# Performance work log

Hardware: AMD Instinct MI355X
Metric: run time of the kernel (lower is better)

## Reference

```python
import jax, jax.numpy as jnp
import numpy as np

EPS = 1e-5

def _layernorm(x, g, b):
    m = jnp.mean(x, axis=-1, keepdims=True)
    v = jnp.mean((x - m) ** 2, axis=-1, keepdims=True)
    return (x - m) * jax.lax.rsqrt(v + EPS) * g + b

def setup_inputs() -> dict:
    key = jax.random.key(0)
    ks = jax.random.split(key, 6)
    b, s, n = 1, 256, 512
    dim_msa, dim_pair, heads, dim_head = 64, 128, 8, 32
    dim_inner = heads * dim_head
    msa = jax.random.normal(ks[0], (b, s, n, dim_msa), dtype=jnp.float32)
    pairwise_repr = jax.random.normal(ks[1], (b, n, n, dim_pair), dtype=jnp.float32)
    mask = jnp.ones((b, n), dtype=bool)
    return {
        "msa": msa,
        "pairwise_repr": pairwise_repr,
        "ln_msa_g": jnp.ones((dim_msa,), jnp.float32),
        "ln_msa_b": jnp.zeros((dim_msa,), jnp.float32),
        "W_vg": jax.random.normal(ks[2], (dim_msa, dim_inner * 2), jnp.float32) * 0.02,
        "ln_pair_g": jnp.ones((dim_pair,), jnp.float32),
        "ln_pair_b": jnp.zeros((dim_pair,), jnp.float32),
        "W_pair": jax.random.normal(ks[3], (dim_pair, heads), jnp.float32) * 0.02,
        "W_out": jax.random.normal(ks[4], (dim_inner, dim_msa), jnp.float32) * 0.02,
        "mask": mask,
    }

def reference(msa, pairwise_repr, ln_msa_g, ln_msa_b, W_vg, ln_pair_g, ln_pair_b, W_pair, W_out, mask):
    heads, dim_head = 8, 32
    b, s, n, dim_msa = msa.shape
    # values and gates: LN -> LinearNoBias -> split (gv h d)
    vg = _layernorm(msa, ln_msa_g, ln_msa_b) @ W_vg            # [b,s,n,2*h*d]
    vg = vg.reshape(b, s, n, 2, heads, dim_head)
    vg = jnp.transpose(vg, (3, 0, 4, 1, 2, 5))                  # [2,b,h,s,n,d]
    values, gates = vg[0], jax.nn.sigmoid(vg[1])
    # pair bias: LN -> LinearNoBias -> [b,h,i,j]
    bias = _layernorm(pairwise_repr, ln_pair_g, ln_pair_b) @ W_pair  # [b,i,j,h]
    bias = jnp.transpose(bias, (0, 3, 1, 2))                    # [b,h,i,j]
    bias = jnp.where(mask[:, None, None, :], bias, -jnp.inf)
    weights = jax.nn.softmax(bias, axis=-1)                     # [b,h,i,j]
    out = jnp.einsum('bhij,bhsjd->bhsid', weights, values)      # [b,h,s,n,d]
    out = out * gates
    out = jnp.transpose(out, (0, 2, 3, 1, 4)).reshape(b, s, n, heads * dim_head)
    return out @ W_out                                          # [b,s,n,dim_msa]
```

## Files before the change

kernel.cpp:

```cpp
#include <hip/hip_runtime.h>
#include <hip/hip_bf16.h>


#define S 256
#define N 512
#define DM 64
#define DP 128
#define H 8
#define C 256
#define ROWS (S * N)

typedef __attribute__((ext_vector_type(8))) short bf16x8;
typedef __attribute__((ext_vector_type(4))) float f32x4;

static __device__ __forceinline__ float bf2f(unsigned int u16) {
    union { unsigned int i; float f; } x;
    x.i = u16 << 16;
    return x.f;
}
static __device__ __forceinline__ unsigned short f2bf(float f) {
    union { float f; unsigned int i; } x;
    x.f = f;
    unsigned int r = x.i + 0x7FFFu + ((x.i >> 16) & 1u);
    return (unsigned short)(r >> 16);
}
static __device__ __forceinline__ void gload16(const void* g, void* l) {
    __builtin_amdgcn_global_load_lds(
        (const __attribute__((address_space(1))) void*)g,
        (__attribute__((address_space(3))) void*)l, 16, 0, 0);
}

__global__ __launch_bounds__(256) void k0_prep(
    const float* __restrict__ Wvg, const float* __restrict__ g, const float* __restrict__ b,
    const float* __restrict__ Wout, const float* __restrict__ gp, const float* __restrict__ bp,
    const float* __restrict__ Wp,
    unsigned short* __restrict__ WTvg, float* __restrict__ biasvg, unsigned short* __restrict__ WoutT,
    float* __restrict__ Wg, float* __restrict__ sgcb)
{
    const int t = threadIdx.x;
    if (blockIdx.x < 2) {
        const int c = blockIdx.x * 256 + t;
        float bias = 0.f;
        unsigned short row[64];
#pragma unroll
        for (int k = 0; k < 64; k++) {
            const float w = Wvg[k * 512 + c];
            row[k] = f2bf(w * g[k]);
            bias = fmaf(w, b[k], bias);
        }
#pragma unroll
        for (int q = 0; q < 8; q++) *(uint4*)(WTvg + c * 64 + q * 8) = *(const uint4*)(row + q * 8);
        biasvg[c] = bias;
    } else if (blockIdx.x == 2) {
        const int m = t >> 2, c0 = (t & 3) * 64;
        unsigned short row[64];
#pragma unroll
        for (int q = 0; q < 64; q++) row[q] = f2bf(Wout[(c0 + q) * 64 + m]);
#pragma unroll
        for (int q = 0; q < 8; q++) *(uint4*)(WoutT + m * 256 + c0 + q * 8) = *(const uint4*)(row + q * 8);
    } else {
        if (t < 128) {
            const float gm = gp[t];
#pragma unroll
            for (int h = 0; h < 8; h++) Wg[t * 8 + h] = gm * Wp[t * 8 + h];
        } else if (t < 136) {
            const int h = t - 128;
            float sg = 0.f, cb = 0.f;
            for (int k = 0; k < 128; k++) {
                sg = fmaf(gp[k], Wp[k * 8 + h], sg);
                cb = fmaf(bp[k], Wp[k * 8 + h], cb);
            }
            sgcb[h] = sg;
            sgcb[8 + h] = cb;
        }
    }
}

__global__ __launch_bounds__(512, 4) void k1_vg_mfma(
    const float* __restrict__ msa, const unsigned short* __restrict__ WTvg,
    const float* __restrict__ biasvg,
    unsigned short* __restrict__ VT, unsigned short* __restrict__ G)
{
    __shared__ unsigned short wt[512 * 64];
    __shared__ unsigned short at[64 * 64];
    const int t = threadIdx.x, lane = t & 63, w = t >> 6;
    const int l15 = lane & 15, lgrp = lane >> 4;
    const int s = blockIdx.x >> 1;
    const int jbase = (blockIdx.x & 1) * 256;

#pragma unroll
    for (int q = 0; q < 8; q++) {
        const int u = q * 512 + t;
        const int c = u >> 3, ch = u & 7;
        const uint4 v = *(const uint4*)(WTvg + c * 64 + ch * 8);
        *(uint4*)((char*)wt + c * 128 + ((ch ^ (c & 7)) * 16)) = v;
    }
    float biasr[4];
    float bias2[4][4];
    if (w < 4) {
#pragma unroll
        for (int cf = 0; cf < 4; cf++) biasr[cf] = biasvg[w * 64 + cf * 16 + l15];
    } else {
#pragma unroll
        for (int cf = 0; cf < 4; cf++)
#pragma unroll
            for (int r = 0; r < 4; r++) bias2[cf][r] = biasvg[w * 64 + cf * 16 + lgrp * 4 + r];
    }

    for (int tile = 0; tile < 4; ++tile) {
        const int j0 = jbase + tile * 64;
        {
            const int r = t >> 3, kc = (t & 7) * 8;
            const float* src = msa + ((size_t)(s * 512 + j0 + r)) * 64 + kc;
            const float4 x0 = *(const float4*)src;
            const float4 x1 = *(const float4*)(src + 4);
            float s1 = x0.x + x0.y + x0.z + x0.w + x1.x + x1.y + x1.z + x1.w;
            float s2 = x0.x * x0.x + x0.y * x0.y + x0.z * x0.z + x0.w * x0.w
                     + x1.x * x1.x + x1.y * x1.y + x1.z * x1.z + x1.w * x1.w;
#pragma unroll
            for (int off = 1; off < 8; off <<= 1) {
                s1 += __shfl_xor(s1, off);
                s2 += __shfl_xor(s2, off);
            }
            const float m = s1 * (1.f / 64.f);
            const float inv = rsqrtf(s2 * (1.f / 64.f) - m * m + 1e-5f);
            unsigned short buf[8];
            buf[0] = f2bf((x0.x - m) * inv); buf[1] = f2bf((x0.y - m) * inv);
            buf[2] = f2bf((x0.z - m) * inv); buf[3] = f2bf((x0.w - m) * inv);
            buf[4] = f2bf((x1.x - m) * inv); buf[5] = f2bf((x1.y - m) * inv);
            buf[6] = f2bf((x1.z - m) * inv); buf[7] = f2bf((x1.w - m) * inv);
            *(uint4*)((char*)at + r * 128 + (((t & 7) ^ (r & 7)) * 16)) = *(const uint4*)buf;
        }
        __syncthreads();

        f32x4 acc[4][4];
#pragma unroll
        for (int rf = 0; rf < 4; rf++)
#pragma unroll
            for (int cf = 0; cf < 4; cf++) acc[rf][cf] = (f32x4){0.f, 0.f, 0.f, 0.f};

#pragma unroll
        for (int ks = 0; ks < 2; ks++) {
            bf16x8 bfr[4];
#pragma unroll
            for (int cf = 0; cf < 4; cf++) {
                const int c = w * 64 + cf * 16 + l15;
                bfr[cf] = *(const bf16x8*)((const char*)wt + c * 128 + (((ks * 4 + lgrp) ^ (c & 7)) * 16));
            }
#pragma unroll
            for (int rf = 0; rf < 4; rf++) {
                const int rr = rf * 16 + l15;
                const bf16x8 afr = *(const bf16x8*)((const char*)at + rr * 128 + (((ks * 4 + lgrp) ^ (rr & 7)) * 16));
                if (w < 4) {
#pragma unroll
                    for (int cf = 0; cf < 4; cf++)
                        acc[rf][cf] = __builtin_amdgcn_mfma_f32_16x16x32_bf16(afr, bfr[cf], acc[rf][cf], 0, 0, 0);
                } else {
#pragma unroll
                    for (int cf = 0; cf < 4; cf++)
                        acc[rf][cf] = __builtin_amdgcn_mfma_f32_16x16x32_bf16(bfr[cf], afr, acc[rf][cf], 0, 0, 0);
                }
            }
        }
        __syncthreads();

        if (w < 4) {
#pragma unroll
            for (int rf = 0; rf < 4; rf++)
#pragma unroll
                for (int cf = 0; cf < 4; cf++) {
                    const int c = w * 64 + cf * 16 + l15;
                    const int j = j0 + rf * 16 + lgrp * 4;
                    uint2 o;
                    o.x = (unsigned)f2bf(acc[rf][cf][0] + biasr[cf]) |
                          ((unsigned)f2bf(acc[rf][cf][1] + biasr[cf]) << 16);
                    o.y = (unsigned)f2bf(acc[rf][cf][2] + biasr[cf]) |
                          ((unsigned)f2bf(acc[rf][cf][3] + biasr[cf]) << 16);
                    *(uint2*)(VT + ((size_t)s * C + c) * N + j) = o;
                }
        } else {
#pragma unroll
            for (int rf = 0; rf < 4; rf++)
#pragma unroll
                for (int cf = 0; cf < 4; cf++) {
                    const int j = j0 + rf * 16 + l15;
                    const int cp = (w - 4) * 64 + cf * 16 + lgrp * 4;
                    float sg[4];
#pragma unroll
                    for (int r = 0; r < 4; r++)
                        sg[r] = 1.f / (1.f + __expf(-(acc[rf][cf][r] + bias2[cf][r])));
                    uint2 o;
                    o.x = (unsigned)f2bf(sg[0]) | ((unsigned)f2bf(sg[1]) << 16);
                    o.y = (unsigned)f2bf(sg[2]) | ((unsigned)f2bf(sg[3]) << 16);
                    *(uint2*)(G + ((size_t)(s * 512 + j)) * C + cp) = o;
                }
        }
    }
}

__global__ __launch_bounds__(512) void k2_bias_softmax(
    const float* __restrict__ pair, const float* __restrict__ Wg,
    const float* __restrict__ sgcb, unsigned short* __restrict__ Wt)
{
    __shared__ float bias_lds[H][N];
    const int i = blockIdx.x;
    const int t = threadIdx.x;
    const int sub = t & 15, rgrp = t >> 4;

    float wreg[2][4][8];
#pragma unroll
    for (int q = 0; q < 2; q++)
#pragma unroll
        for (int c = 0; c < 4; c++) {
            const int k = (q * 16 + sub) * 4 + c;
            const float4 w0 = *(const float4*)(Wg + k * 8);
            const float4 w1 = *(const float4*)(Wg + k * 8 + 4);
            wreg[q][c][0] = w0.x; wreg[q][c][1] = w0.y; wreg[q][c][2] = w0.z; wreg[q][c][3] = w0.w;
            wreg[q][c][4] = w1.x; wreg[q][c][5] = w1.y; wreg[q][c][6] = w1.z; wreg[q][c][7] = w1.w;
        }
    float sgr[8], cbr[8];
#pragma unroll
    for (int h = 0; h < 8; h++) { sgr[h] = sgcb[h]; cbr[h] = sgcb[8 + h]; }

    for (int pass = 0; pass < 16; ++pass) {
        const int r = pass * 32 + rgrp;
        const float* px = pair + ((size_t)i * N + r) * DP;
        const float4 x0 = *(const float4*)(px + (0 * 16 + sub) * 4);
        const float4 x1 = *(const float4*)(px + (1 * 16 + sub) * 4);
        float s1 = x0.x + x0.y + x0.z + x0.w + x1.x + x1.y + x1.z + x1.w;
        float s2 = x0.x * x0.x + x0.y * x0.y + x0.z * x0.z + x0.w * x0.w
                 + x1.x * x1.x + x1.y * x1.y + x1.z * x1.z + x1.w * x1.w;
#pragma unroll
        for (int off = 1; off < 16; off <<= 1) {
            s1 += __shfl_xor(s1, off);
            s2 += __shfl_xor(s2, off);
        }
        const float m = s1 * (1.f / 128.f);
        const float inv = rsqrtf(s2 * (1.f / 128.f) - m * m + 1e-5f);

        float dots[8];
#pragma unroll
        for (int h = 0; h < 8; h++) dots[h] = 0.f;
        const float xs[2][4] = {{x0.x, x0.y, x0.z, x0.w}, {x1.x, x1.y, x1.z, x1.w}};
#pragma unroll
        for (int q = 0; q < 2; q++)
#pragma unroll
            for (int c = 0; c < 4; c++)
#pragma unroll
                for (int h = 0; h < 8; h++) dots[h] = fmaf(xs[q][c], wreg[q][c][h], dots[h]);
#pragma unroll
        for (int off = 1; off < 16; off <<= 1)
#pragma unroll
            for (int h = 0; h < 8; h++) dots[h] += __shfl_xor(dots[h], off);

        if (sub == 0) {
#pragma unroll
            for (int h = 0; h < 8; h++)
                bias_lds[h][r] = inv * (dots[h] - m * sgr[h]) + cbr[h];
        }
    }
    __syncthreads();

    const int lane = t & 63, h = t >> 6;
    float v[8];
    float mx = -1e30f;
#pragma unroll
    for (int q = 0; q < 8; q++) {
        v[q] = bias_lds[h][q * 64 + lane];
        mx = fmaxf(mx, v[q]);
    }
#pragma unroll
    for (int off = 32; off > 0; off >>= 1) mx = fmaxf(mx, __shfl_xor(mx, off));
    float sum = 0.f;
#pragma unroll
    for (int q = 0; q < 8; q++) {
        v[q] = __expf(v[q] - mx);
        sum += v[q];
    }
#pragma unroll
    for (int off = 32; off > 0; off >>= 1) sum += __shfl_xor(sum, off);
    const float rs = 1.f / sum;
#pragma unroll
    for (int q = 0; q < 8; q++)
        Wt[((size_t)h * N + i) * N + q * 64 + lane] = f2bf(v[q] * rs);
}

__global__ __launch_bounds__(256, 2) void k3_einsum_h(
    const unsigned short* __restrict__ Wt, const unsigned short* __restrict__ VT,
    unsigned short* __restrict__ G)
{
    __shared__ unsigned short a_lds[128 * 64];
    __shared__ unsigned short b_lds[256 * 64];
    const int raw = blockIdx.x;
    const int bid = (raw & 7) * 128 + (raw >> 3);
    const int h = bid >> 7;
    const int rem = bid & 127;
    const int nb = rem >> 1, ib = rem & 1;
    const int n0 = nb * 128, i0 = ib * 256;
    const int t = threadIdx.x, lane = t & 63, w = t >> 6;
    const int l15 = lane & 15, lgrp = lane >> 4;
    const int wn = w >> 1, wi = w & 1;

    const unsigned short* srcA[4];
    const unsigned short* srcB[8];
    int dstA[4], dstB[8];
#pragma unroll
    for (int q = 0; q < 4; ++q) {
        const int slot = q * 256 + t;
        const int row = slot >> 3, chp = slot & 7;
        const int ch = chp ^ (row & 7);
        const int n = n0 + row;
        srcA[q] = VT + ((size_t)((n >> 5) * 256 + h * 32 + (n & 31))) * 512 + ch * 8;
        dstA[q] = slot * 16;
    }
#pragma unroll
    for (int q = 0; q < 8; ++q) {
        const int slot = q * 256 + t;
        const int row = slot >> 3, chp = slot & 7;
        const int ch = chp ^ (row & 7);
        srcB[q] = Wt + ((size_t)(h * 512 + i0 + row)) * 512 + ch * 8;
        dstB[q] = slot * 16;
    }

    f32x4 acc[4][8];
#pragma unroll
    for (int fn = 0; fn < 4; fn++)
#pragma unroll
        for (int fi = 0; fi < 8; fi++) acc[fn][fi] = (f32x4){0.f, 0.f, 0.f, 0.f};

    for (int kt = 0; kt < 8; ++kt) {
        const int j0 = kt * 64;
#pragma unroll
        for (int q = 0; q < 4; ++q) gload16(srcA[q] + j0, (char*)a_lds + dstA[q]);
#pragma unroll
        for (int q = 0; q < 8; ++q) gload16(srcB[q] + j0, (char*)b_lds + dstB[q]);
        __syncthreads();

#pragma unroll
        for (int ks = 0; ks < 2; ++ks) {
            bf16x8 af[4];
#pragma unroll
            for (int fn = 0; fn < 4; ++fn) {
                const int ra = wn * 64 + fn * 16 + l15;
                af[fn] = *(const bf16x8*)((const char*)a_lds + ra * 128 + (((ks * 4 + lgrp) ^ (ra & 7)) * 16));
            }
            bf16x8 bf[8];
#pragma unroll
            for (int fi = 0; fi < 8; ++fi) {
                const int rb = wi * 128 + fi * 16 + l15;
                bf[fi] = *(const bf16x8*)((const char*)b_lds + rb * 128 + (((ks * 4 + lgrp) ^ (rb & 7)) * 16));
            }
#pragma unroll
            for (int fn = 0; fn < 4; ++fn)
#pragma unroll
                for (int fi = 0; fi < 8; ++fi)
                    acc[fn][fi] = __builtin_amdgcn_mfma_f32_16x16x32_bf16(af[fn], bf[fi], acc[fn][fi], 0, 0, 0);
        }
        __syncthreads();
    }

#pragma unroll
    for (int fn = 0; fn < 4; ++fn) {
        const int nl = n0 + wn * 64 + fn * 16 + lgrp * 4;
        const int s = nl >> 5, d = nl & 31;
#pragma unroll
        for (int fi = 0; fi < 8; ++fi) {
            const int i = i0 + wi * 128 + fi * 16 + l15;
            const size_t base = ((size_t)(s * 512 + i)) * 256 + h * 32 + d;
            const uint2 uu = *(const uint2*)(G + base);
            const float g0 = bf2f(uu.x & 0xFFFFu), g1 = bf2f(uu.x >> 16);
            const float g2 = bf2f(uu.y & 0xFFFFu), g3 = bf2f(uu.y >> 16);
            uint2 o;
            o.x = (unsigned)f2bf(acc[fn][fi][0] * g0) | ((unsigned)f2bf(acc[fn][fi][1] * g1) << 16);
            o.y = (unsigned)f2bf(acc[fn][fi][2] * g2) | ((unsigned)f2bf(acc[fn][fi][3] * g3) << 16);
            *(uint2*)(G + base) = o;
        }
    }
}

__global__ __launch_bounds__(256, 4) void k4_out(
    const unsigned short* __restrict__ gated, const unsigned short* __restrict__ WoutT,
    float* __restrict__ out)
{
    __shared__ unsigned short w_lds[64 * 256];
    __shared__ unsigned short a_lds[64 * 256];
    const int t = threadIdx.x, lane = t & 63, w = t >> 6;
    const int l15 = lane & 15, lgrp = lane >> 4;
    const size_t r0 = (size_t)blockIdx.x * 64;

#pragma unroll
    for (int q = 0; q < 8; ++q) {
        const int u = q * 256 + t;
        const int row = u >> 5, kc = u & 31;
        const uint4 v = *(const uint4*)(WoutT + row * 256 + kc * 8);
        *(uint4*)((char*)w_lds + row * 512 + ((kc ^ (row & 31)) * 16)) = v;
    }
#pragma unroll
    for (int q = 0; q < 8; ++q) {
        const int slot = q * 256 + t;
        const int row = slot >> 5, chp = slot & 31;
        const int ch = chp ^ (row & 31);
        gload16(gated + (r0 + row) * 256 + ch * 8,
                (char*)a_lds + (q * 256 + (t & 192)) * 16);
    }
    __syncthreads();

    f32x4 acc[4];
#pragma unroll
    for (int fm = 0; fm < 4; fm++) acc[fm] = (f32x4){0.f, 0.f, 0.f, 0.f};
#pragma unroll
    for (int ks = 0; ks < 8; ++ks) {
        const int ra = w * 16 + l15;
        const bf16x8 af = *(const bf16x8*)((const char*)a_lds + ra * 512 + (((ks * 4 + lgrp) ^ (ra & 31)) * 16));
#pragma unroll
        for (int fm = 0; fm < 4; ++fm) {
            const int rm = fm * 16 + l15;
            const bf16x8 bf = *(const bf16x8*)((const char*)w_lds + rm * 512 + (((ks * 4 + lgrp) ^ (rm & 31)) * 16));
            acc[fm] = __builtin_amdgcn_mfma_f32_16x16x32_bf16(af, bf, acc[fm], 0, 0, 0);
        }
    }
#pragma unroll
    for (int fm = 0; fm < 4; ++fm)
#pragma unroll
        for (int r = 0; r < 4; ++r)
            out[(r0 + w * 16 + lgrp * 4 + r) * 64 + fm * 16 + l15] = acc[fm][r];
}

extern "C" void kernel_launch(void* const* d_in, const int* in_sizes, int n_in,
                              void* d_out, int out_size, void* d_ws, size_t ws_size,
                              hipStream_t stream) {
    (void)in_sizes; (void)n_in; (void)out_size; (void)ws_size;
    const float* msa       = (const float*)d_in[0];
    const float* pair      = (const float*)d_in[1];
    const float* ln_msa_g  = (const float*)d_in[2];
    const float* ln_msa_b  = (const float*)d_in[3];
    const float* W_vg      = (const float*)d_in[4];
    const float* ln_pair_g = (const float*)d_in[5];
    const float* ln_pair_b = (const float*)d_in[6];
    const float* W_pair    = (const float*)d_in[7];
    const float* W_out     = (const float*)d_in[8];
    float* out = (float*)d_out;

    char* ws = (char*)d_ws;
    size_t off = 0;
    unsigned short* VT    = (unsigned short*)(ws + off); off += (size_t)ROWS * C * 2;
    unsigned short* G     = (unsigned short*)(ws + off); off += (size_t)ROWS * C * 2;
    unsigned short* Wt    = (unsigned short*)(ws + off); off += (size_t)H * N * N * 2;
    unsigned short* WTvg  = (unsigned short*)(ws + off); off += 512 * 64 * 2;
    float*          biasvg = (float*)(ws + off); off += 512 * 4;
    unsigned short* WoutT = (unsigned short*)(ws + off); off += 64 * 256 * 2;
    float*          Wg    = (float*)(ws + off); off += 128 * 8 * 4;
    float*          sgcb  = (float*)(ws + off); off += 16 * 4;

    k0_prep<<<4, 256, 0, stream>>>(W_vg, ln_msa_g, ln_msa_b, W_out, ln_pair_g, ln_pair_b, W_pair,
                                   WTvg, biasvg, WoutT, Wg, sgcb);
    k2_bias_softmax<<<512, 512, 0, stream>>>(pair, Wg, sgcb, Wt);
    k1_vg_mfma<<<512, 512, 0, stream>>>(msa, WTvg, biasvg, VT, G);
    k3_einsum_h<<<1024, 256, 0, stream>>>(Wt, VT, G);
    k4_out<<<2048, 256, 0, stream>>>(G, WoutT, out);
}
```

Baseline: 227.0 us.

## Fuse head-wise einsum, gating and output projection into one kernel

Merges the per-head weights×values GEMM, the gate multiply and the W_out projection into one kernel. Each block now owns 2 s-rows by 128 i-rows and loops over all 8 heads, staging the gated tile in LDS and accumulating the output projection in registers. This removes the write of the gated tensor to global memory and its read-back in a separate kernel, plus one launch. The cost is smaller GEMM tiles with less reuse, fewer blocks (512 instead of 1024), extra syncs per head and more register pressure.

```diff
diff --git a/kernel.cpp b/kernel.cpp
--- a/kernel.cpp
+++ b/kernel.cpp
@@ -285,145 +285,144 @@
         Wt[((size_t)h * N + i) * N + q * 64 + lane] = f2bf(v[q] * rs);
 }
 
-__global__ __launch_bounds__(256, 2) void k3_einsum_h(
+__global__ __launch_bounds__(256, 2) void k3_fused_out(
     const unsigned short* __restrict__ Wt, const unsigned short* __restrict__ VT,
-    unsigned short* __restrict__ G)
+    const unsigned short* __restrict__ G, const unsigned short* __restrict__ WoutT,
+    float* __restrict__ out)
 {
-    __shared__ unsigned short a_lds[128 * 64];
-    __shared__ unsigned short b_lds[256 * 64];
+    __shared__ unsigned short a_lds[64 * 64];
+    __shared__ unsigned short b_lds[128 * 64];
+    __shared__ unsigned short g_lds[2 * 128 * 32];
     const int raw = blockIdx.x;
-    const int bid = (raw & 7) * 128 + (raw >> 3);
-    const int h = bid >> 7;
-    const int rem = bid & 127;
-    const int nb = rem >> 1, ib = rem & 1;
-    const int n0 = nb * 128, i0 = ib * 256;
+    const int bid = (raw & 7) * 64 + (raw >> 3);
+    const int sp = bid >> 2;
+    const int it = bid & 3;
+    const int s0 = sp * 2, i0 = it * 128;
     const int t = threadIdx.x, lane = t & 63, w = t >> 6;
     const int l15 = lane & 15, lgrp = lane >> 4;
     const int wn = w >> 1, wi = w & 1;
 
-    const unsigned short* srcA[4];
-    const unsigned short* srcB[8];
-    int dstA[4], dstB[8];
+    const unsigned short* srcA[2];
+    const unsigned short* srcB[4];
+    int dstA[2], dstB[4];
+#pragma unroll
+    for (int q = 0; q < 2; ++q) {
+        const int slot = q * 256 + t;
+        const int row = slot >> 3, chp = slot & 7;
+        const int ch = chp ^ (row & 7);
+        srcA[q] = VT + ((size_t)((s0 + (row >> 5)) * 256 + (row & 31))) * 512 + ch * 8;
+        dstA[q] = slot * 16;
+    }
 #pragma unroll
     for (int q = 0; q < 4; ++q) {
         const int slot = q * 256 + t;
         const int row = slot >> 3, chp = slot & 7;
         const int ch = chp ^ (row & 7);
-        const int n = n0 + row;
-        srcA[q] = VT + ((size_t)((n >> 5) * 256 + h * 32 + (n & 31))) * 512 + ch * 8;
-        dstA[q] = slot * 16;
-    }
-#pragma unroll
-    for (int q = 0; q < 8; ++q) {
-        const int slot = q * 256 + t;
-        const int row = slot >> 3, chp = slot & 7;
-        const int ch = chp ^ (row & 7);
-        srcB[q] = Wt + ((size_t)(h * 512 + i0 + row)) * 512 + ch * 8;
+        srcB[q] = Wt + ((size_t)(i0 + row)) * 512 + ch * 8;
         dstB[q] = slot * 16;
     }
 
-    f32x4 acc[4][8];
-#pragma unroll
-    for (int fn = 0; fn < 4; fn++)
-#pragma unroll
-        for (int fi = 0; fi < 8; fi++) acc[fn][fi] = (f32x4){0.f, 0.f, 0.f, 0.f};
-
-    for (int kt = 0; kt < 8; ++kt) {
-        const int j0 = kt * 64;
-#pragma unroll
-        for (int q = 0; q < 4; ++q) gload16(srcA[q] + j0, (char*)a_lds + dstA[q]);
-#pragma unroll
-        for (int q = 0; q < 8; ++q) gload16(srcB[q] + j0, (char*)b_lds + dstB[q]);
+    f32x4 oacc[2][2][4];
+#pragma unroll
+    for (int s = 0; s < 2; s++)
+#pragma unroll
+        for (int f = 0; f < 2; f++)
+#pragma unroll
+            for (int mf = 0; mf < 4; mf++) oacc[s][f][mf] = (f32x4){0.f, 0.f, 0.f, 0.f};
+
+    for (int h = 0; h < 8; ++h) {
+        uint2 gpre[2][4];
+#pragma unroll
+        for (int fn = 0; fn < 2; ++fn)
+#pragma unroll
+            for (int fi = 0; fi < 4; ++fi)
+                gpre[fn][fi] = *(const uint2*)(G +
+                    ((size_t)((s0 + wn) * 512 + i0 + wi * 64 + fi * 16 + l15)) * 256 +
+                    h * 32 + fn * 16 + lgrp * 4);
+
+        f32x4 acc[2][4];
+#pragma unroll
+        for (int fn = 0; fn < 2; fn++)
+#pragma unroll
+            for (int fi = 0; fi < 4; fi++) acc[fn][fi] = (f32x4){0.f, 0.f, 0.f, 0.f};
+
+        const int offA = h * 16384;
+        const int offB = h * 262144;
+        for (int kt = 0; kt < 8; ++kt) {
+            const int j0 = kt * 64;
+#pragma unroll
+            for (int q = 0; q < 2; ++q) gload16(srcA[q] + offA + j0, (char*)a_lds + dstA[q]);
+#pragma unroll
+            for (int q = 0; q < 4; ++q) gload16(srcB[q] + offB + j0, (char*)b_lds + dstB[q]);
+            __syncthreads();
+#pragma unroll
+            for (int ks = 0; ks < 2; ++ks) {
+                bf16x8 af[2], bf[4];
+#pragma unroll
+                for (int fn = 0; fn < 2; ++fn) {
+                    const int ra = wn * 32 + fn * 16 + l15;
+                    af[fn] = *(const bf16x8*)((const char*)a_lds + ra * 128 + (((ks * 4 + lgrp) ^ (ra & 7)) * 16));
+                }
+#pragma unroll
+                for (int fi = 0; fi < 4; ++fi) {
+                    const int rb = wi * 64 + fi * 16 + l15;
+                    bf[fi] = *(const bf16x8*)((const char*)b_lds + rb * 128 + (((ks * 4 + lgrp) ^ (rb & 7)) * 16));
+                }
+#pragma unroll
+                for (int fn = 0; fn < 2; ++fn)
+#pragma unroll
+                    for (int fi = 0; fi < 4; ++fi)
+                        acc[fn][fi] = __builtin_amdgcn_mfma_f32_16x16x32_bf16(af[fn], bf[fi], acc[fn][fi], 0, 0, 0);
+            }
+            __syncthreads();
+        }
+
+#pragma unroll
+        for (int fn = 0; fn < 2; ++fn) {
+            const int d0 = fn * 16 + lgrp * 4;
+#pragma unroll
+            for (int fi = 0; fi < 4; ++fi) {
+                const int i = wi * 64 + fi * 16 + l15;
+                const uint2 uu = gpre[fn][fi];
+                const float g0 = bf2f(uu.x & 0xFFFFu), g1 = bf2f(uu.x >> 16);
+                const float g2 = bf2f(uu.y & 0xFFFFu), g3 = bf2f(uu.y >> 16);
+                uint2 o;
+                o.x = (unsigned)f2bf(acc[fn][fi][0] * g0) | ((unsigned)f2bf(acc[fn][fi][1] * g1) << 16);
+                o.y = (unsigned)f2bf(acc[fn][fi][2] * g2) | ((unsigned)f2bf(acc[fn][fi][3] * g3) << 16);
+                *(uint2*)((char*)g_lds + wn * 8192 + i * 64 + (((d0 >> 3) ^ (i & 3)) * 16) + (d0 & 7) * 2) = o;
+            }
+        }
         __syncthreads();
 
-#pragma unroll
-        for (int ks = 0; ks < 2; ++ks) {
-            bf16x8 af[4];
-#pragma unroll
-            for (int fn = 0; fn < 4; ++fn) {
-                const int ra = wn * 64 + fn * 16 + l15;
-                af[fn] = *(const bf16x8*)((const char*)a_lds + ra * 128 + (((ks * 4 + lgrp) ^ (ra & 7)) * 16));
-            }
-            bf16x8 bf[8];
-#pragma unroll
-            for (int fi = 0; fi < 8; ++fi) {
-                const int rb = wi * 128 + fi * 16 + l15;
-                bf[fi] = *(const bf16x8*)((const char*)b_lds + rb * 128 + (((ks * 4 + lgrp) ^ (rb & 7)) * 16));
-            }
-#pragma unroll
-            for (int fn = 0; fn < 4; ++fn)
-#pragma unroll
-                for (int fi = 0; fi < 8; ++fi)
-                    acc[fn][fi] = __builtin_amdgcn_mfma_f32_16x16x32_bf16(af[fn], bf[fi], acc[fn][fi], 0, 0, 0);
+        bf16x8 bw[4];
+#pragma unroll
+        for (int mf = 0; mf < 4; ++mf)
+            bw[mf] = *(const bf16x8*)(WoutT + (mf * 16 + l15) * 256 + h * 32 + lgrp * 8);
+#pragma unroll
+        for (int s = 0; s < 2; ++s) {
+#pragma unroll
+            for (int f = 0; f < 2; ++f) {
+                const int ra = w * 32 + f * 16 + l15;
+                const bf16x8 af = *(const bf16x8*)((const char*)g_lds + s * 8192 + ra * 64 + ((lgrp ^ (ra & 3)) * 16));
+#pragma unroll
+                for (int mf = 0; mf < 4; ++mf)
+                    oacc[s][f][mf] = __builtin_amdgcn_mfma_f32_16x16x32_bf16(af, bw[mf], oacc[s][f][mf], 0, 0, 0);
+            }
         }
         __syncthreads();
     }
 
 #pragma unroll
-    for (int fn = 0; fn < 4; ++fn) {
-        const int nl = n0 + wn * 64 + fn * 16 + lgrp * 4;
-        const int s = nl >> 5, d = nl & 31;
-#pragma unroll
-        for (int fi = 0; fi < 8; ++fi) {
-            const int i = i0 + wi * 128 + fi * 16 + l15;
-            const size_t base = ((size_t)(s * 512 + i)) * 256 + h * 32 + d;
-            const uint2 uu = *(const uint2*)(G + base);
-            const float g0 = bf2f(uu.x & 0xFFFFu), g1 = bf2f(uu.x >> 16);
-            const float g2 = bf2f(uu.y & 0xFFFFu), g3 = bf2f(uu.y >> 16);
-            uint2 o;
-            o.x = (unsigned)f2bf(acc[fn][fi][0] * g0) | ((unsigned)f2bf(acc[fn][fi][1] * g1) << 16);
-            o.y = (unsigned)f2bf(acc[fn][fi][2] * g2) | ((unsigned)f2bf(acc[fn][fi][3] * g3) << 16);
-            *(uint2*)(G + base) = o;
-        }
-    }
-}
-
-__global__ __launch_bounds__(256, 4) void k4_out(
-    const unsigned short* __restrict__ gated, const unsigned short* __restrict__ WoutT,
-    float* __restrict__ out)
-{
-    __shared__ unsigned short w_lds[64 * 256];
-    __shared__ unsigned short a_lds[64 * 256];
-    const int t = threadIdx.x, lane = t & 63, w = t >> 6;
-    const int l15 = lane & 15, lgrp = lane >> 4;
-    const size_t r0 = (size_t)blockIdx.x * 64;
-
-#pragma unroll
-    for (int q = 0; q < 8; ++q) {
-        const int u = q * 256 + t;
-        const int row = u >> 5, kc = u & 31;
-        const uint4 v = *(const uint4*)(WoutT + row * 256 + kc * 8);
-        *(uint4*)((char*)w_lds + row * 512 + ((kc ^ (row & 31)) * 16)) = v;
-    }
-#pragma unroll
-    for (int q = 0; q < 8; ++q) {
-        const int slot = q * 256 + t;
-        const int row = slot >> 5, chp = slot & 31;
-        const int ch = chp ^ (row & 31);
-        gload16(gated + (r0 + row) * 256 + ch * 8,
-                (char*)a_lds + (q * 256 + (t & 192)) * 16);
-    }
-    __syncthreads();
-
-    f32x4 acc[4];
-#pragma unroll
-    for (int fm = 0; fm < 4; fm++) acc[fm] = (f32x4){0.f, 0.f, 0.f, 0.f};
-#pragma unroll
-    for (int ks = 0; ks < 8; ++ks) {
-        const int ra = w * 16 + l15;
-        const bf16x8 af = *(const bf16x8*)((const char*)a_lds + ra * 512 + (((ks * 4 + lgrp) ^ (ra & 31)) * 16));
-#pragma unroll
-        for (int fm = 0; fm < 4; ++fm) {
-            const int rm = fm * 16 + l15;
-            const bf16x8 bf = *(const bf16x8*)((const char*)w_lds + rm * 512 + (((ks * 4 + lgrp) ^ (rm & 31)) * 16));
-            acc[fm] = __builtin_amdgcn_mfma_f32_16x16x32_bf16(af, bf, acc[fm], 0, 0, 0);
-        }
-    }
-#pragma unroll
-    for (int fm = 0; fm < 4; ++fm)
-#pragma unroll
-        for (int r = 0; r < 4; ++r)
-            out[(r0 + w * 16 + lgrp * 4 + r) * 64 + fm * 16 + l15] = acc[fm][r];
+    for (int s = 0; s < 2; ++s)
+#pragma unroll
+        for (int f = 0; f < 2; ++f)
+#pragma unroll
+            for (int mf = 0; mf < 4; ++mf)
+#pragma unroll
+                for (int r = 0; r < 4; ++r) {
+                    const size_t row = (size_t)(s0 + s) * 512 + i0 + w * 32 + f * 16 + lgrp * 4 + r;
+                    out[row * 64 + mf * 16 + l15] = oacc[s][f][mf][r];
+                }
 }
 
 extern "C" void kernel_launch(void* const* d_in, const int* in_sizes, int n_in,
@@ -456,6 +455,5 @@
                                    WTvg, biasvg, WoutT, Wg, sgcb);
     k2_bias_softmax<<<512, 512, 0, stream>>>(pair, Wg, sgcb, Wt);
     k1_vg_mfma<<<512, 512, 0, stream>>>(msa, WTvg, biasvg, VT, G);
-    k3_einsum_h<<<1024, 256, 0, stream>>>(Wt, VT, G);
-    k4_out<<<2048, 256, 0, stream>>>(G, WoutT, out);
-}
+    k3_fused_out<<<512, 256, 0, stream>>>(Wt, VT, G, WoutT, out);
+}
```

Measured after the change: 203.5 us. 1.12x faster.
